# Kernel optimization log

Hardware: AMD Instinct MI355X
Metric: run time of the kernel (lower is better)

## Reference

```python
import jax, jax.numpy as jnp
import numpy as np

D_MODEL = 1024
NUM_HEADS = 16
D_K = D_MODEL // NUM_HEADS  # 64


def setup_inputs() -> dict:
    key = jax.random.key(0)
    ks = jax.random.split(key, 9)
    B, S = 4, 2048
    scale = 1.0 / np.sqrt(D_MODEL)
    x = jax.random.normal(ks[0], (B, S, D_MODEL), dtype=jnp.float32)
    Wq = jax.random.normal(ks[1], (D_MODEL, D_MODEL), dtype=jnp.float32) * scale
    Wk = jax.random.normal(ks[2], (D_MODEL, D_MODEL), dtype=jnp.float32) * scale
    Wv = jax.random.normal(ks[3], (D_MODEL, D_MODEL), dtype=jnp.float32) * scale
    Wo = jax.random.normal(ks[4], (D_MODEL, D_MODEL), dtype=jnp.float32) * scale
    bq = jax.random.normal(ks[5], (D_MODEL,), dtype=jnp.float32) * 0.01
    bk = jax.random.normal(ks[6], (D_MODEL,), dtype=jnp.float32) * 0.01
    bv = jax.random.normal(ks[7], (D_MODEL,), dtype=jnp.float32) * 0.01
    bo = jax.random.normal(ks[8], (D_MODEL,), dtype=jnp.float32) * 0.01
    return {"x": x, "Wq": Wq, "bq": bq, "Wk": Wk, "bk": bk,
            "Wv": Wv, "bv": bv, "Wo": Wo, "bo": bo}


def reference(x, Wq, bq, Wk, bk, Wv, bv, Wo, bo):
    B, S, D = x.shape
    H, dk = NUM_HEADS, D_K
    # QKV projections, split into heads: [B, H, S, dk]
    def heads(W, b):
        return (x @ W + b).reshape(B, S, H, dk).transpose(0, 2, 1, 3)
    q = heads(Wq, bq)
    k = heads(Wk, bk)
    v = heads(Wv, bv)
    # scaled dot-product attention
    scores = jnp.einsum("bhqd,bhkd->bhqk", q, k) / jnp.sqrt(jnp.float32(dk))
    attn = jax.nn.softmax(scores, axis=-1)
    ctx = jnp.einsum("bhqk,bhkd->bhqd", attn, v)  # [B,H,S,dk]
    ctx = ctx.transpose(0, 2, 1, 3).reshape(B, S, D)
    return ctx @ Wo + bo
```

## Files before the change

kernel.cpp:

```cpp
#include <hip/hip_runtime.h>
#include <hip/hip_bf16.h>


#define MH_B 4
#define MH_S 2048
#define MH_D 1024
#define MH_H 16
#define MH_DK 64

typedef __bf16 bf16_t;
typedef bf16_t bf16x8 __attribute__((ext_vector_type(8)));
typedef bf16_t bf16x4 __attribute__((ext_vector_type(4)));
typedef float  f32x4  __attribute__((ext_vector_type(4)));

__global__ __launch_bounds__(256) void convert_bf16_kernel(
    const float* __restrict__ in, bf16_t* __restrict__ out, int n4)
{
    for (int i = blockIdx.x * 256 + threadIdx.x; i < n4; i += gridDim.x * 256) {
        float4 v = ((const float4*)in)[i];
        bf16x4 o;
        o[0] = (bf16_t)v.x; o[1] = (bf16_t)v.y;
        o[2] = (bf16_t)v.z; o[3] = (bf16_t)v.w;
        ((bf16x4*)out)[i] = o;
    }
}

__global__ __launch_bounds__(256) void transpose_w_kernel(
    const float* __restrict__ W0, const float* __restrict__ W1,
    const float* __restrict__ W2, const float* __restrict__ W3,
    bf16_t* __restrict__ out)
{
    const float* W = (blockIdx.z == 0) ? W0 : (blockIdx.z == 1) ? W1
                   : (blockIdx.z == 2) ? W2 : W3;
    bf16_t* O = out + (size_t)blockIdx.z * MH_D * MH_D;
    __shared__ float T[32][33];
    const int tx = threadIdx.x, ty = threadIdx.y;
    const int k0 = blockIdx.y * 32, n0 = blockIdx.x * 32;
#pragma unroll
    for (int i = 0; i < 4; ++i)
        T[ty + i * 8][tx] = W[(size_t)(k0 + ty + i * 8) * MH_D + n0 + tx];
    __syncthreads();
#pragma unroll
    for (int i = 0; i < 4; ++i)
        O[(size_t)(n0 + ty + i * 8) * MH_D + k0 + tx] = (bf16_t)T[tx][ty + i * 8];
}

template<int MODE>
__global__ __launch_bounds__(256) void gemm_mfma_kernel(
    const bf16_t* __restrict__ A, const bf16_t* __restrict__ Bt,
    const float* __restrict__ bias, void* __restrict__ Cout,
    int M, int N, int K)
{
    __shared__ bf16_t As[128 * 64];
    __shared__ bf16_t Bs[128 * 64];

    const int tid = threadIdx.x;
    const int lane = tid & 63, wid = tid >> 6;
    const int lr = lane & 15, lg = lane >> 4;
    const int wr = wid >> 1, wc = wid & 1;
    const int bm = blockIdx.y * 128, bn = blockIdx.x * 128;

    const int srow = tid >> 1;
    const int sbase = (tid & 1) * 4;
    const int r7 = srow & 7;
    const int wbase = srow * 64;

    const bf16_t* Ag = A + (size_t)(bm + srow) * K;
    const bf16_t* Bg = Bt + (size_t)(bn + srow) * K;

    f32x4 acc[4][4];
#pragma unroll
    for (int i = 0; i < 4; ++i)
#pragma unroll
        for (int j = 0; j < 4; ++j) acc[i][j] = (f32x4){0.f, 0.f, 0.f, 0.f};

    bf16x8 ra[4], rb[4];
#pragma unroll
    for (int u = 0; u < 4; ++u) {
        ra[u] = *(const bf16x8*)&Ag[(sbase + u) * 8];
        rb[u] = *(const bf16x8*)&Bg[(sbase + u) * 8];
    }
#pragma unroll
    for (int u = 0; u < 4; ++u) {
        *(bf16x8*)&As[wbase + (((sbase + u) ^ r7) << 3)] = ra[u];
        *(bf16x8*)&Bs[wbase + (((sbase + u) ^ r7) << 3)] = rb[u];
    }
    __syncthreads();

    const int nk = K >> 6;
    for (int kt = 0; kt < nk; ++kt) {
        const bool pf = (kt + 1 < nk);
        if (pf) {
            const int k0 = (kt + 1) << 6;
#pragma unroll
            for (int u = 0; u < 4; ++u) {
                ra[u] = *(const bf16x8*)&Ag[k0 + (sbase + u) * 8];
                rb[u] = *(const bf16x8*)&Bg[k0 + (sbase + u) * 8];
            }
        }
#pragma unroll
        for (int kc = 0; kc < 2; ++kc) {
            bf16x8 af[4], bfr[4];
#pragma unroll
            for (int i = 0; i < 4; ++i) {
                const int arow = wr * 64 + i * 16 + lr;
                af[i] = *(const bf16x8*)&As[arow * 64 + ((((kc << 2) + lg) ^ (lr & 7)) << 3)];
                const int brow = wc * 64 + i * 16 + lr;
                bfr[i] = *(const bf16x8*)&Bs[brow * 64 + ((((kc << 2) + lg) ^ (lr & 7)) << 3)];
            }
#pragma unroll
            for (int i = 0; i < 4; ++i)
#pragma unroll
                for (int j = 0; j < 4; ++j)
                    acc[i][j] = __builtin_amdgcn_mfma_f32_16x16x32_bf16(
                        af[i], bfr[j], acc[i][j], 0, 0, 0);
        }
        __syncthreads();
        if (pf) {
#pragma unroll
            for (int u = 0; u < 4; ++u) {
                *(bf16x8*)&As[wbase + (((sbase + u) ^ r7) << 3)] = ra[u];
                *(bf16x8*)&Bs[wbase + (((sbase + u) ^ r7) << 3)] = rb[u];
            }
        }
        __syncthreads();
    }

#pragma unroll
    for (int j = 0; j < 4; ++j) {
        const int n = bn + wc * 64 + j * 16 + lr;
        const float bj = bias[n];
#pragma unroll
        for (int i = 0; i < 4; ++i) {
            const int m0 = bm + wr * 64 + i * 16 + (lg << 2);
            if (MODE == 0) {
                bf16_t* C = (bf16_t*)Cout;
#pragma unroll
                for (int r = 0; r < 4; ++r)
                    C[(size_t)(m0 + r) * N + n] = (bf16_t)(acc[i][j][r] + bj);
            } else if (MODE == 1) {
                float* C = (float*)Cout;
#pragma unroll
                for (int r = 0; r < 4; ++r)
                    C[(size_t)(m0 + r) * N + n] = acc[i][j][r] + bj;
            } else {
                bf16_t* C = (bf16_t*)Cout;
                const int h = n >> 6, d = n & 63;
                const int bb = m0 >> 11, s0 = m0 & 2047;
                bf16x4 pk;
#pragma unroll
                for (int r = 0; r < 4; ++r) pk[r] = (bf16_t)(acc[i][j][r] + bj);
                *(bf16x4*)&C[(((size_t)(bb * MH_H + h) * MH_DK + d) << 11) + s0] = pk;
            }
        }
    }
}

__global__ __launch_bounds__(256) void attn_mfma_kernel(
    const bf16_t* __restrict__ Q, const bf16_t* __restrict__ Kg_,
    const bf16_t* __restrict__ Vt, bf16_t* __restrict__ ctx)
{
    __shared__ bf16_t Ks[64 * 64];
    __shared__ bf16_t Vs[64 * 64];
    __shared__ bf16_t Ps[4 * 16 * 64];

    const int tid = threadIdx.x;
    const int lane = tid & 63, wid = tid >> 6;
    const int lr = lane & 15, lg = lane >> 4;
    const int h = blockIdx.x & 15, b = blockIdx.x >> 4;
    const int qt = blockIdx.y;

    const size_t qtok = (size_t)(b * MH_S + qt * 64 + wid * 16 + lr);
    bf16x8 qf[2];
    qf[0] = *(const bf16x8*)&Q[qtok * MH_D + h * 64 + (lg << 3)];
    qf[1] = *(const bf16x8*)&Q[qtok * MH_D + h * 64 + 32 + (lg << 3)];

    const int srow = tid >> 2;
    const int sb = (tid & 3) * 2;
    const int r7 = srow & 7;
    const int wbase = srow * 64;
    const bf16_t* Kgp = Kg_ + (size_t)(b * MH_S) * MH_D + h * 64 + (size_t)srow * MH_D;
    const bf16_t* Vgp = Vt + ((size_t)(b * MH_H + h) * MH_DK + srow) * MH_S;

    f32x4 oacc[4];
#pragma unroll
    for (int nf = 0; nf < 4; ++nf) oacc[nf] = (f32x4){0.f, 0.f, 0.f, 0.f};
    float mrun[4] = {-1e30f, -1e30f, -1e30f, -1e30f};
    float lrun[4] = {0.f, 0.f, 0.f, 0.f};

    bf16x8 rk[2], rv[2];
#pragma unroll
    for (int u = 0; u < 2; ++u) {
        rk[u] = *(const bf16x8*)&Kgp[(sb + u) * 8];
        rv[u] = *(const bf16x8*)&Vgp[(sb + u) * 8];
    }
#pragma unroll
    for (int u = 0; u < 2; ++u) {
        *(bf16x8*)&Ks[wbase + (((sb + u) ^ r7) << 3)] = rk[u];
        *(bf16x8*)&Vs[wbase + (((sb + u) ^ r7) << 3)] = rv[u];
    }
    __syncthreads();

    const int pbase = wid * 1024;
    for (int kt = 0; kt < MH_S / 64; ++kt) {
        const bool pf = (kt + 1 < MH_S / 64);
        if (pf) {
            const int kv0 = (kt + 1) * 64;
#pragma unroll
            for (int u = 0; u < 2; ++u) {
                rk[u] = *(const bf16x8*)&Kgp[(size_t)kv0 * MH_D + (sb + u) * 8];
                rv[u] = *(const bf16x8*)&Vgp[kv0 + (sb + u) * 8];
            }
        }

        f32x4 sc[4];
#pragma unroll
        for (int j = 0; j < 4; ++j) sc[j] = (f32x4){0.f, 0.f, 0.f, 0.f};
#pragma unroll
        for (int kc = 0; kc < 2; ++kc) {
            const int sl = (((kc << 2) + lg) ^ (lr & 7)) << 3;
#pragma unroll
            for (int j = 0; j < 4; ++j) {
                bf16x8 kf = *(const bf16x8*)&Ks[(j * 16 + lr) * 64 + sl];
                sc[j] = __builtin_amdgcn_mfma_f32_16x16x32_bf16(qf[kc], kf, sc[j], 0, 0, 0);
            }
        }

        float rmx[4];
#pragma unroll
        for (int j = 0; j < 4; ++j) sc[j] *= 0.125f;
#pragma unroll
        for (int r = 0; r < 4; ++r)
            rmx[r] = fmaxf(fmaxf(sc[0][r], sc[1][r]), fmaxf(sc[2][r], sc[3][r]));
#pragma unroll
        for (int off = 1; off < 16; off <<= 1)
#pragma unroll
            for (int r = 0; r < 4; ++r)
                rmx[r] = fmaxf(rmx[r], __shfl_xor(rmx[r], off));

        float fsc[4];
#pragma unroll
        for (int r = 0; r < 4; ++r) {
            const float mn = fmaxf(mrun[r], rmx[r]);
            fsc[r] = __expf(mrun[r] - mn);
            mrun[r] = mn;
        }
        float rsum[4] = {0.f, 0.f, 0.f, 0.f};
#pragma unroll
        for (int j = 0; j < 4; ++j)
#pragma unroll
            for (int r = 0; r < 4; ++r) {
                const float p = __expf(sc[j][r] - mrun[r]);
                rsum[r] += p;
                const int ql = (lg << 2) + r;
                const int key = j * 16 + lr;
                Ps[pbase + ql * 64 + ((((key >> 3) ^ (ql & 7)) << 3)) + (key & 7)] = (bf16_t)p;
            }
#pragma unroll
        for (int off = 1; off < 16; off <<= 1)
#pragma unroll
            for (int r = 0; r < 4; ++r) rsum[r] += __shfl_xor(rsum[r], off);
#pragma unroll
        for (int r = 0; r < 4; ++r) lrun[r] = lrun[r] * fsc[r] + rsum[r];
        f32x4 fv = {fsc[0], fsc[1], fsc[2], fsc[3]};
#pragma unroll
        for (int nf = 0; nf < 4; ++nf) oacc[nf] *= fv;

#pragma unroll
        for (int kc = 0; kc < 2; ++kc) {
            const int sl = (((kc << 2) + lg) ^ (lr & 7)) << 3;
            bf16x8 pa = *(const bf16x8*)&Ps[pbase + lr * 64 + sl];
#pragma unroll
            for (int nf = 0; nf < 4; ++nf) {
                bf16x8 vf = *(const bf16x8*)&Vs[(nf * 16 + lr) * 64 + sl];
                oacc[nf] = __builtin_amdgcn_mfma_f32_16x16x32_bf16(pa, vf, oacc[nf], 0, 0, 0);
            }
        }

        __syncthreads();
        if (pf) {
#pragma unroll
            for (int u = 0; u < 2; ++u) {
                *(bf16x8*)&Ks[wbase + (((sb + u) ^ r7) << 3)] = rk[u];
                *(bf16x8*)&Vs[wbase + (((sb + u) ^ r7) << 3)] = rv[u];
            }
        }
        __syncthreads();
    }

    float inv[4];
#pragma unroll
    for (int r = 0; r < 4; ++r) inv[r] = 1.f / lrun[r];
#pragma unroll
    for (int nf = 0; nf < 4; ++nf)
#pragma unroll
        for (int r = 0; r < 4; ++r) {
            const int token = qt * 64 + wid * 16 + (lg << 2) + r;
            const int d = nf * 16 + lr;
            ctx[(size_t)(b * MH_S + token) * MH_D + h * 64 + d] =
                (bf16_t)(oacc[nf][r] * inv[r]);
        }
}

extern "C" void kernel_launch(void* const* d_in, const int* in_sizes, int n_in,
                              void* d_out, int out_size, void* d_ws, size_t ws_size,
                              hipStream_t stream) {
    const float* x  = (const float*)d_in[0];
    const float* Wq = (const float*)d_in[1];
    const float* bq = (const float*)d_in[2];
    const float* Wk = (const float*)d_in[3];
    const float* bk = (const float*)d_in[4];
    const float* Wv = (const float*)d_in[5];
    const float* bv = (const float*)d_in[6];
    const float* Wo = (const float*)d_in[7];
    const float* bo = (const float*)d_in[8];

    const int M = MH_B * MH_S;
    const int N = MH_D;
    const int K = MH_D;

    char* ws = (char*)d_ws;
    bf16_t* xb  = (bf16_t*)(ws);
    bf16_t* Wt  = (bf16_t*)(ws + (size_t)16 * 1048576);
    bf16_t* Qb  = (bf16_t*)(ws + (size_t)24 * 1048576);
    bf16_t* Kb  = (bf16_t*)(ws + (size_t)40 * 1048576);
    bf16_t* Vtb = (bf16_t*)(ws + (size_t)56 * 1048576);
    bf16_t* ctx = (bf16_t*)(ws + (size_t)72 * 1048576);

    hipLaunchKernelGGL(convert_bf16_kernel, dim3(2048), dim3(256), 0, stream,
                       x, xb, M * K / 4);
    hipLaunchKernelGGL(transpose_w_kernel, dim3(32, 32, 4), dim3(32, 8), 0, stream,
                       Wq, Wk, Wv, Wo, Wt);

    const size_t WSTRIDE = (size_t)MH_D * MH_D;
    dim3 gg(N / 128, M / 128);
    hipLaunchKernelGGL(gemm_mfma_kernel<0>, gg, dim3(256), 0, stream,
                       xb, Wt + 0 * WSTRIDE, bq, (void*)Qb, M, N, K);
    hipLaunchKernelGGL(gemm_mfma_kernel<0>, gg, dim3(256), 0, stream,
                       xb, Wt + 1 * WSTRIDE, bk, (void*)Kb, M, N, K);
    hipLaunchKernelGGL(gemm_mfma_kernel<2>, gg, dim3(256), 0, stream,
                       xb, Wt + 2 * WSTRIDE, bv, (void*)Vtb, M, N, K);

    hipLaunchKernelGGL(attn_mfma_kernel, dim3(MH_B * MH_H, MH_S / 64), dim3(256),
                       0, stream, Qb, Kb, Vtb, ctx);

    hipLaunchKernelGGL(gemm_mfma_kernel<1>, gg, dim3(256), 0, stream,
                       ctx, Wt + 3 * WSTRIDE, bo, d_out, M, N, K);
}
```

Baseline: 416.5 us.

## Use direct global-to-LDS loads in GEMM and widen attention KV tiles

The GEMM drops the register-staged, double-buffered prefetch and the XOR swizzle. It loads tiles with global_load_lds straight into unswizzled shared memory, and reorders workgroups so neighbouring tiles share cached data. The attention kernel doubles the KV block to 128 and swaps the score MFMA operands so each lane owns a single query row, which cuts the shuffle reductions. It also pre-scales Q by 1/sqrt(dk) and writes P as packed 4-element vectors. The intent is to reduce register traffic and softmax overhead, but the GEMM now has no load/compute overlap and may suffer LDS bank conflicts on its unswizzled reads.

```diff
diff --git a/kernel.cpp b/kernel.cpp
--- a/kernel.cpp
+++ b/kernel.cpp
@@ -12,6 +12,12 @@
 typedef bf16_t bf16x8 __attribute__((ext_vector_type(8)));
 typedef bf16_t bf16x4 __attribute__((ext_vector_type(4)));
 typedef float  f32x4  __attribute__((ext_vector_type(4)));
+
+__device__ __forceinline__ void gll16(const void* g, void* l) {
+    __builtin_amdgcn_global_load_lds(
+        (__attribute__((address_space(1))) void*)const_cast<void*>(g),
+        (__attribute__((address_space(3))) void*)l, 16, 0, 0);
+}
 
 __global__ __launch_bounds__(256) void convert_bf16_kernel(
     const float* __restrict__ in, bf16_t* __restrict__ out, int n4)
@@ -58,55 +64,41 @@
     const int lane = tid & 63, wid = tid >> 6;
     const int lr = lane & 15, lg = lane >> 4;
     const int wr = wid >> 1, wc = wid & 1;
-    const int bm = blockIdx.y * 128, bn = blockIdx.x * 128;
-
-    const int srow = tid >> 1;
-    const int sbase = (tid & 1) * 4;
-    const int r7 = srow & 7;
-    const int wbase = srow * 64;
-
-    const bf16_t* Ag = A + (size_t)(bm + srow) * K;
-    const bf16_t* Bg = Bt + (size_t)(bn + srow) * K;
+
+    const int nx = gridDim.x;
+    const int wg = blockIdx.y * nx + blockIdx.x;
+    const int cpx = (nx * gridDim.y) >> 3;
+    const int swz = (wg & 7) * cpx + (wg >> 3);
+    const int bm = (swz / nx) * 128;
+    const int bn = (swz % nx) * 128;
+
+    const int crow = lane >> 3;
+    const int cslot = lane & 7;
 
     f32x4 acc[4][4];
 #pragma unroll
     for (int i = 0; i < 4; ++i)
 #pragma unroll
         for (int j = 0; j < 4; ++j) acc[i][j] = (f32x4){0.f, 0.f, 0.f, 0.f};
-
-    bf16x8 ra[4], rb[4];
-#pragma unroll
-    for (int u = 0; u < 4; ++u) {
-        ra[u] = *(const bf16x8*)&Ag[(sbase + u) * 8];
-        rb[u] = *(const bf16x8*)&Bg[(sbase + u) * 8];
-    }
-#pragma unroll
-    for (int u = 0; u < 4; ++u) {
-        *(bf16x8*)&As[wbase + (((sbase + u) ^ r7) << 3)] = ra[u];
-        *(bf16x8*)&Bs[wbase + (((sbase + u) ^ r7) << 3)] = rb[u];
-    }
-    __syncthreads();
 
     const int nk = K >> 6;
     for (int kt = 0; kt < nk; ++kt) {
-        const bool pf = (kt + 1 < nk);
-        if (pf) {
-            const int k0 = (kt + 1) << 6;
-#pragma unroll
-            for (int u = 0; u < 4; ++u) {
-                ra[u] = *(const bf16x8*)&Ag[k0 + (sbase + u) * 8];
-                rb[u] = *(const bf16x8*)&Bg[k0 + (sbase + u) * 8];
-            }
-        }
+        const int k0 = kt << 6;
+#pragma unroll
+        for (int u = 0; u < 4; ++u) {
+            const int c = wid * 4 + u;
+            const int row = c * 8 + crow;
+            gll16(&A[(size_t)(bm + row) * K + k0 + cslot * 8], &As[c * 512]);
+            gll16(&Bt[(size_t)(bn + row) * K + k0 + cslot * 8], &Bs[c * 512]);
+        }
+        __syncthreads();
 #pragma unroll
         for (int kc = 0; kc < 2; ++kc) {
             bf16x8 af[4], bfr[4];
 #pragma unroll
             for (int i = 0; i < 4; ++i) {
-                const int arow = wr * 64 + i * 16 + lr;
-                af[i] = *(const bf16x8*)&As[arow * 64 + ((((kc << 2) + lg) ^ (lr & 7)) << 3)];
-                const int brow = wc * 64 + i * 16 + lr;
-                bfr[i] = *(const bf16x8*)&Bs[brow * 64 + ((((kc << 2) + lg) ^ (lr & 7)) << 3)];
+                af[i]  = *(const bf16x8*)&As[(wr * 64 + i * 16 + lr) * 64 + ((kc << 2) + lg) * 8];
+                bfr[i] = *(const bf16x8*)&Bs[(wc * 64 + i * 16 + lr) * 64 + ((kc << 2) + lg) * 8];
             }
 #pragma unroll
             for (int i = 0; i < 4; ++i)
@@ -114,14 +106,6 @@
                 for (int j = 0; j < 4; ++j)
                     acc[i][j] = __builtin_amdgcn_mfma_f32_16x16x32_bf16(
                         af[i], bfr[j], acc[i][j], 0, 0, 0);
-        }
-        __syncthreads();
-        if (pf) {
-#pragma unroll
-            for (int u = 0; u < 4; ++u) {
-                *(bf16x8*)&As[wbase + (((sbase + u) ^ r7) << 3)] = ra[u];
-                *(bf16x8*)&Bs[wbase + (((sbase + u) ^ r7) << 3)] = rb[u];
-            }
         }
         __syncthreads();
     }
@@ -156,17 +140,21 @@
     }
 }
 
+#define KVB 128
+#define NKT (MH_S / KVB)
+
 __global__ __launch_bounds__(256) void attn_mfma_kernel(
     const bf16_t* __restrict__ Q, const bf16_t* __restrict__ Kg_,
     const bf16_t* __restrict__ Vt, bf16_t* __restrict__ ctx)
 {
-    __shared__ bf16_t Ks[64 * 64];
-    __shared__ bf16_t Vs[64 * 64];
-    __shared__ bf16_t Ps[4 * 16 * 64];
+    __shared__ bf16_t Ks[KVB * 64];
+    __shared__ bf16_t Vs[64 * KVB];
+    __shared__ bf16_t Ps[4 * 16 * KVB];
 
     const int tid = threadIdx.x;
     const int lane = tid & 63, wid = tid >> 6;
     const int lr = lane & 15, lg = lane >> 4;
+    const int l7 = lr & 7;
     const int h = blockIdx.x & 15, b = blockIdx.x >> 4;
     const int qt = blockIdx.y;
 
@@ -174,105 +162,104 @@
     bf16x8 qf[2];
     qf[0] = *(const bf16x8*)&Q[qtok * MH_D + h * 64 + (lg << 3)];
     qf[1] = *(const bf16x8*)&Q[qtok * MH_D + h * 64 + 32 + (lg << 3)];
-
-    const int srow = tid >> 2;
-    const int sb = (tid & 3) * 2;
-    const int r7 = srow & 7;
-    const int wbase = srow * 64;
-    const bf16_t* Kgp = Kg_ + (size_t)(b * MH_S) * MH_D + h * 64 + (size_t)srow * MH_D;
-    const bf16_t* Vgp = Vt + ((size_t)(b * MH_H + h) * MH_DK + srow) * MH_S;
+#pragma unroll
+    for (int kc = 0; kc < 2; ++kc)
+#pragma unroll
+        for (int e = 0; e < 8; ++e)
+            qf[kc][e] = (bf16_t)(0.125f * (float)qf[kc][e]);
+
+    const int krow = tid >> 1, ks0 = (tid & 1) << 2;
+    const int vrow = tid >> 2, vs0 = (tid & 3) << 2;
+    const bf16_t* Kgp = Kg_ + ((size_t)(b * MH_S) + krow) * MH_D + h * 64;
+    const bf16_t* Vgp = Vt + ((size_t)(b * MH_H + h) * MH_DK + vrow) * MH_S;
 
     f32x4 oacc[4];
 #pragma unroll
     for (int nf = 0; nf < 4; ++nf) oacc[nf] = (f32x4){0.f, 0.f, 0.f, 0.f};
-    float mrun[4] = {-1e30f, -1e30f, -1e30f, -1e30f};
-    float lrun[4] = {0.f, 0.f, 0.f, 0.f};
-
-    bf16x8 rk[2], rv[2];
-#pragma unroll
-    for (int u = 0; u < 2; ++u) {
-        rk[u] = *(const bf16x8*)&Kgp[(sb + u) * 8];
-        rv[u] = *(const bf16x8*)&Vgp[(sb + u) * 8];
-    }
-#pragma unroll
-    for (int u = 0; u < 2; ++u) {
-        *(bf16x8*)&Ks[wbase + (((sb + u) ^ r7) << 3)] = rk[u];
-        *(bf16x8*)&Vs[wbase + (((sb + u) ^ r7) << 3)] = rv[u];
+    float mrun = -1e30f, lrun = 0.f;
+
+    bf16x8 rk[4], rv[4];
+#pragma unroll
+    for (int u = 0; u < 4; ++u) {
+        rk[u] = *(const bf16x8*)&Kgp[(ks0 + u) * 8];
+        rv[u] = *(const bf16x8*)&Vgp[(vs0 + u) * 8];
+    }
+#pragma unroll
+    for (int u = 0; u < 4; ++u) {
+        *(bf16x8*)&Ks[krow * 64 + (((ks0 + u) ^ (krow & 7)) << 3)] = rk[u];
+        *(bf16x8*)&Vs[vrow * KVB + (((vs0 + u) ^ (vrow & 7)) << 3)] = rv[u];
     }
     __syncthreads();
 
-    const int pbase = wid * 1024;
-    for (int kt = 0; kt < MH_S / 64; ++kt) {
-        const bool pf = (kt + 1 < MH_S / 64);
+    const int pbase = wid * (16 * KVB);
+
+    for (int kt = 0; kt < NKT; ++kt) {
+        const bool pf = (kt + 1 < NKT);
         if (pf) {
-            const int kv0 = (kt + 1) * 64;
-#pragma unroll
-            for (int u = 0; u < 2; ++u) {
-                rk[u] = *(const bf16x8*)&Kgp[(size_t)kv0 * MH_D + (sb + u) * 8];
-                rv[u] = *(const bf16x8*)&Vgp[kv0 + (sb + u) * 8];
-            }
-        }
-
-        f32x4 sc[4];
-#pragma unroll
-        for (int j = 0; j < 4; ++j) sc[j] = (f32x4){0.f, 0.f, 0.f, 0.f};
+            const int kv0 = (kt + 1) * KVB;
+#pragma unroll
+            for (int u = 0; u < 4; ++u) {
+                rk[u] = *(const bf16x8*)&Kgp[(size_t)kv0 * MH_D + (ks0 + u) * 8];
+                rv[u] = *(const bf16x8*)&Vgp[kv0 + (vs0 + u) * 8];
+            }
+        }
+
+        f32x4 sc[8];
+#pragma unroll
+        for (int j = 0; j < 8; ++j) sc[j] = (f32x4){0.f, 0.f, 0.f, 0.f};
 #pragma unroll
         for (int kc = 0; kc < 2; ++kc) {
-            const int sl = (((kc << 2) + lg) ^ (lr & 7)) << 3;
-#pragma unroll
-            for (int j = 0; j < 4; ++j) {
+            const int sl = (((kc << 2) + lg) ^ l7) << 3;
+#pragma unroll
+            for (int j = 0; j < 8; ++j) {
                 bf16x8 kf = *(const bf16x8*)&Ks[(j * 16 + lr) * 64 + sl];
-                sc[j] = __builtin_amdgcn_mfma_f32_16x16x32_bf16(qf[kc], kf, sc[j], 0, 0, 0);
-            }
-        }
-
-        float rmx[4];
-#pragma unroll
-        for (int j = 0; j < 4; ++j) sc[j] *= 0.125f;
-#pragma unroll
-        for (int r = 0; r < 4; ++r)
-            rmx[r] = fmaxf(fmaxf(sc[0][r], sc[1][r]), fmaxf(sc[2][r], sc[3][r]));
-#pragma unroll
-        for (int off = 1; off < 16; off <<= 1)
-#pragma unroll
-            for (int r = 0; r < 4; ++r)
-                rmx[r] = fmaxf(rmx[r], __shfl_xor(rmx[r], off));
-
-        float fsc[4];
-#pragma unroll
-        for (int r = 0; r < 4; ++r) {
-            const float mn = fmaxf(mrun[r], rmx[r]);
-            fsc[r] = __expf(mrun[r] - mn);
-            mrun[r] = mn;
-        }
-        float rsum[4] = {0.f, 0.f, 0.f, 0.f};
-#pragma unroll
-        for (int j = 0; j < 4; ++j)
-#pragma unroll
-            for (int r = 0; r < 4; ++r) {
-                const float p = __expf(sc[j][r] - mrun[r]);
-                rsum[r] += p;
-                const int ql = (lg << 2) + r;
-                const int key = j * 16 + lr;
-                Ps[pbase + ql * 64 + ((((key >> 3) ^ (ql & 7)) << 3)) + (key & 7)] = (bf16_t)p;
-            }
-#pragma unroll
-        for (int off = 1; off < 16; off <<= 1)
-#pragma unroll
-            for (int r = 0; r < 4; ++r) rsum[r] += __shfl_xor(rsum[r], off);
-#pragma unroll
-        for (int r = 0; r < 4; ++r) lrun[r] = lrun[r] * fsc[r] + rsum[r];
-        f32x4 fv = {fsc[0], fsc[1], fsc[2], fsc[3]};
+                sc[j] = __builtin_amdgcn_mfma_f32_16x16x32_bf16(kf, qf[kc], sc[j], 0, 0, 0);
+            }
+        }
+
+        float pmax = -1e30f;
+#pragma unroll
+        for (int j = 0; j < 8; ++j) {
+            pmax = fmaxf(pmax, fmaxf(fmaxf(sc[j][0], sc[j][1]),
+                                     fmaxf(sc[j][2], sc[j][3])));
+        }
+        pmax = fmaxf(pmax, __shfl_xor(pmax, 16));
+        pmax = fmaxf(pmax, __shfl_xor(pmax, 32));
+        const float mn = fmaxf(mrun, pmax);
+        const float fsc = __expf(mrun - mn);
+        mrun = mn;
+
+        float rsum = 0.f;
+#pragma unroll
+        for (int j = 0; j < 8; ++j) {
+            const float p0 = __expf(sc[j][0] - mn);
+            const float p1 = __expf(sc[j][1] - mn);
+            const float p2 = __expf(sc[j][2] - mn);
+            const float p3 = __expf(sc[j][3] - mn);
+            rsum += (p0 + p1) + (p2 + p3);
+            bf16x4 p4;
+            p4[0] = (bf16_t)p0; p4[1] = (bf16_t)p1;
+            p4[2] = (bf16_t)p2; p4[3] = (bf16_t)p3;
+            const int slot = (2 * j + (lg >> 1)) ^ l7;
+            *(bf16x4*)&Ps[pbase + lr * KVB + (slot << 3) + ((lg & 1) << 2)] = p4;
+        }
+        rsum += __shfl_xor(rsum, 16);
+        rsum += __shfl_xor(rsum, 32);
+        lrun = lrun * fsc + rsum;
+
+        f32x4 fv;
+#pragma unroll
+        for (int r = 0; r < 4; ++r) fv[r] = __shfl(fsc, (lg << 2) | r);
 #pragma unroll
         for (int nf = 0; nf < 4; ++nf) oacc[nf] *= fv;
 
 #pragma unroll
-        for (int kc = 0; kc < 2; ++kc) {
-            const int sl = (((kc << 2) + lg) ^ (lr & 7)) << 3;
-            bf16x8 pa = *(const bf16x8*)&Ps[pbase + lr * 64 + sl];
+        for (int kc = 0; kc < 4; ++kc) {
+            const int sl = (((kc << 2) + lg) ^ l7) << 3;
+            bf16x8 pa = *(const bf16x8*)&Ps[pbase + lr * KVB + sl];
 #pragma unroll
             for (int nf = 0; nf < 4; ++nf) {
-                bf16x8 vf = *(const bf16x8*)&Vs[(nf * 16 + lr) * 64 + sl];
+                bf16x8 vf = *(const bf16x8*)&Vs[(nf * 16 + lr) * KVB + sl];
                 oacc[nf] = __builtin_amdgcn_mfma_f32_16x16x32_bf16(pa, vf, oacc[nf], 0, 0, 0);
             }
         }
@@ -280,25 +267,24 @@
         __syncthreads();
         if (pf) {
 #pragma unroll
-            for (int u = 0; u < 2; ++u) {
-                *(bf16x8*)&Ks[wbase + (((sb + u) ^ r7) << 3)] = rk[u];
-                *(bf16x8*)&Vs[wbase + (((sb + u) ^ r7) << 3)] = rv[u];
+            for (int u = 0; u < 4; ++u) {
+                *(bf16x8*)&Ks[krow * 64 + (((ks0 + u) ^ (krow & 7)) << 3)] = rk[u];
+                *(bf16x8*)&Vs[vrow * KVB + (((vs0 + u) ^ (vrow & 7)) << 3)] = rv[u];
             }
         }
         __syncthreads();
     }
 
-    float inv[4];
-#pragma unroll
-    for (int r = 0; r < 4; ++r) inv[r] = 1.f / lrun[r];
+    f32x4 linv;
+#pragma unroll
+    for (int r = 0; r < 4; ++r) linv[r] = 1.f / __shfl(lrun, (lg << 2) | r);
 #pragma unroll
     for (int nf = 0; nf < 4; ++nf)
 #pragma unroll
         for (int r = 0; r < 4; ++r) {
             const int token = qt * 64 + wid * 16 + (lg << 2) + r;
-            const int d = nf * 16 + lr;
-            ctx[(size_t)(b * MH_S + token) * MH_D + h * 64 + d] =
-                (bf16_t)(oacc[nf][r] * inv[r]);
+            ctx[(size_t)(b * MH_S + token) * MH_D + h * 64 + nf * 16 + lr] =
+                (bf16_t)(oacc[nf][r] * linv[r]);
         }
 }
 
```

Result: faster. 350.1 us (-15.9%).
